# Performance work log

Measured on AMD Instinct MI355X. Metric: run time of the kernel, lower is better.

Reference implementation:

```python
import jax, jax.numpy as jnp
import numpy as np
from jax import lax

K = 3
STRIDE = 1
PAD = 1


def setup_inputs() -> dict:
    key = jax.random.key(0)
    k1, k2, k3, k4 = jax.random.split(key, 4)
    x = jax.random.normal(k1, (8, 64, 128, 128), dtype=jnp.float32)
    # offset conv params (trained-state stand-in; module inits to 0, which is degenerate)
    w_off = jax.random.normal(k2, (2 * K * K, 64, K, K), dtype=jnp.float32) * 0.01
    b_off = jax.random.normal(k3, (2 * K * K,), dtype=jnp.float32) * 0.01
    w_dcn = jax.random.normal(k4, (64, 64, K, K), dtype=jnp.float32) * 0.05
    return {"x": x, "w_off": w_off, "b_off": b_off, "w_dcn": w_dcn}


def _deform_conv(x, offset, weight):
    # x: [B,C,H,W]; offset: [B,2*K*K,Ho,Wo] interleaved (dy,dx) per kernel tap;
    # weight: [Cout,Cin,K,K]. Matches torchvision.ops.deform_conv2d semantics (groups=1).
    B, C, H, W = x.shape
    Cout = weight.shape[0]
    KK = K * K
    Ho = (H + 2 * PAD - K) // STRIDE + 1
    Wo = (W + 2 * PAD - K) // STRIDE + 1
    off = offset.reshape(B, KK, 2, Ho, Wo)
    ky = (jnp.arange(KK) // K).astype(x.dtype)
    kx = (jnp.arange(KK) % K).astype(x.dtype)
    base_y = (jnp.arange(Ho) * STRIDE - PAD).astype(x.dtype)
    base_x = (jnp.arange(Wo) * STRIDE - PAD).astype(x.dtype)
    # sampling coords per (batch, kernel tap, output y, output x)
    py = base_y[None, None, :, None] + ky[None, :, None, None] + off[:, :, 0]  # [B,KK,Ho,Wo]
    px = base_x[None, None, None, :] + kx[None, :, None, None] + off[:, :, 1]
    y0 = jnp.floor(py)
    x0 = jnp.floor(px)
    dy = py - y0
    dx = px - x0
    y0i = y0.astype(jnp.int32)
    x0i = x0.astype(jnp.int32)
    flat = x.reshape(B, C, H * W)

    def gather(yi, xi):
        valid = (yi >= 0) & (yi < H) & (xi >= 0) & (xi < W)
        idx = (jnp.clip(yi, 0, H - 1) * W + jnp.clip(xi, 0, W - 1)).reshape(B, -1)
        g = jax.vmap(lambda f, i: f[:, i])(flat, idx)  # [B,C,KK*Ho*Wo]
        return g.reshape(B, C, KK, Ho, Wo) * valid.reshape(B, 1, KK, Ho, Wo).astype(x.dtype)

    w00 = ((1 - dy) * (1 - dx))[:, None]  # [B,1,KK,Ho,Wo]
    w01 = ((1 - dy) * dx)[:, None]
    w10 = (dy * (1 - dx))[:, None]
    w11 = (dy * dx)[:, None]
    vals = (gather(y0i, x0i) * w00 + gather(y0i, x0i + 1) * w01
            + gather(y0i + 1, x0i) * w10 + gather(y0i + 1, x0i + 1) * w11)
    return jnp.einsum('bckhw,ock->bohw', vals, weight.reshape(Cout, C, KK))


def reference(x, w_off, b_off, w_dcn):
    offset = lax.conv_general_dilated(
        x, w_off, window_strides=(STRIDE, STRIDE),
        padding=((PAD, PAD), (PAD, PAD)),
        dimension_numbers=('NCHW', 'OIHW', 'NCHW')) + b_off[None, :, None, None]
    return _deform_conv(x, offset, w_dcn)
```

## Files before the change

kernel.cpp:

```cpp
#include <hip/hip_runtime.h>
#include <cmath>

#define BATCH 8
#define CIN   64
#define HH    128
#define WW    128
#define COUT  64
#define KKT   9
#define NOFF  18
#define PIX   16
#define NPX   32
#define KTOT  576
#define WROWS 6
#define WCOLS 24
#define NSAMP (NPX*KKT)
#define KH3   192

typedef __bf16 bf16x8 __attribute__((ext_vector_type(8)));
typedef float  f32x4  __attribute__((ext_vector_type(4)));
typedef float  f32x2  __attribute__((ext_vector_type(2)));
typedef unsigned int u32;
typedef u32    u32x4  __attribute__((ext_vector_type(4)));

__device__ __bf16 g_wb[18 * 4 * 4 * 16 * 8];
__device__ __bf16 g_wboff[18 * 2 * 4 * 16 * 8];

__global__ __launch_bounds__(256)
void prep_w(const float* __restrict__ w_dcn, const float* __restrict__ w_off) {
    const int idx = blockIdx.x * 256 + threadIdx.x;
    if (idx < 18 * 4 * 4 * 16 * 8) {
        const int e  = idx & 7;
        const int lr = (idx >> 3) & 15;
        const int lg = (idx >> 7) & 3;
        const int w  = (idx >> 9) & 3;
        const int kb = idx >> 11;
        const int cout = w * 16 + lr;
        const int k  = kb * 32 + lg * 8 + e;
        const int kk = k >> 6, ci = k & 63;
        g_wb[idx] = (__bf16)w_dcn[cout * KTOT + ci * KKT + kk];
    } else {
        const int j  = idx - 18 * 4 * 4 * 16 * 8;
        const int e  = j & 7;
        const int lr = (j >> 3) & 15;
        const int lg = (j >> 7) & 3;
        const int nt = (j >> 9) & 1;
        const int kb = j >> 10;
        const int oc = nt * 16 + lr;
        const int k  = kb * 32 + lg * 8 + e;
        const int kk = k >> 6, ci = k & 63;
        g_wboff[j] = (oc < NOFF) ? (__bf16)w_off[oc * KTOT + ci * KKT + kk] : (__bf16)0.f;
    }
}

static __device__ __forceinline__ f32x2 unpk(u32 v) {
    f32x2 r;
    r.x = __builtin_bit_cast(float, v << 16);
    r.y = __builtin_bit_cast(float, v & 0xffff0000u);
    return r;
}

__global__ __launch_bounds__(256)
void deform_fused(const float* __restrict__ x,
                  const float* __restrict__ b_off,
                  float* __restrict__ out) {
    __shared__ __align__(16) __bf16 s_xw[WROWS * WCOLS * 64];
    __shared__ __align__(16) __bf16 s_vals[NPX * KH3];
    __shared__ float s_off[NPX * NOFF];
    __shared__ int   s_yx[NSAMP];
    __shared__ float s_bw[NSAMP][4];
    __shared__ int   s_fast[NSAMP];

    const int blk   = blockIdx.x;
    const int wtile = blk % (WW / PIX);
    const int r0    = ((blk / (WW / PIX)) % (HH / 2)) * 2;
    const int b     = blk / ((WW / PIX) * (HH / 2));
    const int wbase = wtile * PIX;
    const int tid   = threadIdx.x;
    const int wid   = tid >> 6;
    const int lane  = tid & 63;
    const int lr    = lane & 15;
    const int lg    = lane >> 4;

    const float* __restrict__ xb = x + (size_t)b * CIN * HH * WW;
    const bool interior = (r0 >= 2) & (r0 <= HH - 4) & (wtile >= 1) & (wtile <= (WW / PIX) - 2);

    for (int t = tid; t < 6 * 64 * WROWS; t += 256) {
        const int c  = t % 6;
        const int ci = (t / 6) & 63;
        const int yr = t / 384;
        const int y  = r0 - 2 + yr;
        const int xs = wbase - 4 + c * 4;
        float v0 = 0.f, v1 = 0.f, v2 = 0.f, v3 = 0.f;
        if (interior) {
            const float* __restrict__ rp = xb + (size_t)ci * (HH * WW) + y * WW + xs;
            const f32x4 v = *(const f32x4*)rp;
            v0 = v[0]; v1 = v[1]; v2 = v[2]; v3 = v[3];
        } else if (y >= 0 && y < HH) {
            const float* __restrict__ rp = xb + (size_t)ci * (HH * WW) + y * WW + xs;
            if (xs >= 0 && xs <= WW - 4) {
                const f32x4 v = *(const f32x4*)rp;
                v0 = v[0]; v1 = v[1]; v2 = v[2]; v3 = v[3];
            } else {
                if (xs + 0 >= 0 && xs + 0 < WW) v0 = rp[0];
                if (xs + 1 >= 0 && xs + 1 < WW) v1 = rp[1];
                if (xs + 2 >= 0 && xs + 2 < WW) v2 = rp[2];
                if (xs + 3 >= 0 && xs + 3 < WW) v3 = rp[3];
            }
        }
        const int eb = ((yr * WCOLS + c * 4) << 6) + ci;
        s_xw[(eb + 0 * 64) ^ (((c * 4 + 0) & 7) << 3)] = (__bf16)v0;
        s_xw[(eb + 1 * 64) ^ (((c * 4 + 1) & 7) << 3)] = (__bf16)v1;
        s_xw[(eb + 2 * 64) ^ (((c * 4 + 2) & 7) << 3)] = (__bf16)v2;
        s_xw[(eb + 3 * 64) ^ (((c * 4 + 3) & 7) << 3)] = (__bf16)v3;
    }
    __syncthreads();

    {
        const int pg = wid >> 1;
        const int nt = wid & 1;
        f32x4 acc = {0.f, 0.f, 0.f, 0.f};
        #pragma unroll
        for (int kb = 0; kb < 18; ++kb) {
            const int kbase = kb * 32 + lg * 8;
            const int kk    = kbase >> 6;
            const int ci0   = kbase & 63;
            const int yr    = pg + kk / 3 + 1;
            const int xr    = lr + kk % 3 + 3;
            const int elem  = (((yr * WCOLS + xr) << 6) + ci0) ^ ((xr & 7) << 3);
            const bf16x8 a  = *(const bf16x8*)&s_xw[elem];
            const bf16x8 bb = *(const bf16x8*)&g_wboff[(((kb * 2 + nt) * 4 + lg) * 16 + lr) * 8];
            acc = __builtin_amdgcn_mfma_f32_16x16x32_bf16(a, bb, acc, 0, 0, 0);
        }
        const int oc = nt * 16 + lr;
        if (oc < NOFF) {
            const float bias = b_off[oc];
            #pragma unroll
            for (int r = 0; r < 4; ++r)
                s_off[(pg * 16 + lg * 4 + r) * NOFF + oc] = acc[r] + bias;
        }
    }
    __syncthreads();

    for (int m = tid; m < NSAMP; m += 256) {
        const int p  = m / KKT;
        const int kk = m - p * KKT;
        const int hp = r0 + (p >> 4);
        const int wo = wbase + (p & 15);
        const float py = (float)(hp - 1 + kk / 3) + s_off[p * NOFF + 2 * kk + 0];
        const float px = (float)(wo - 1 + kk % 3) + s_off[p * NOFF + 2 * kk + 1];
        const float fy = floorf(py), fx = floorf(px);
        const int y0 = (int)fy, x0 = (int)fx;
        const float dy = py - fy, dx = px - fx;
        s_yx[m] = (y0 << 16) | (x0 & 0xffff);
        s_fast[m] = (y0 >= r0 - 2) & (y0 <= r0 + 2) &
                    (x0 >= wbase - 4) & (x0 <= wbase + 18);
        s_bw[m][0] = (1.f - dy) * (1.f - dx);
        s_bw[m][1] = (1.f - dy) * dx;
        s_bw[m][2] = dy * (1.f - dx);
        s_bw[m][3] = dy * dx;
    }
    __syncthreads();

    auto run_task = [&](int m, int p, int kkl, int c8) {
        const int yx = s_yx[m];
        const int y0 = yx >> 16;
        const int x0 = (int)(short)(yx & 0xffff);
        const f32x4 w = *(const f32x4*)&s_bw[m][0];
        bf16x8 o;
        if (s_fast[m]) {
            const int yr  = y0 - (r0 - 2);
            const int xr  = x0 - (wbase - 4);
            const int e00 = ((yr * WCOLS + xr) << 6) + c8;
            const int sw0 = (xr & 7) << 3;
            const int sw1 = ((xr + 1) & 7) << 3;
            const u32x4 u00 = *(const u32x4*)&s_xw[e00 ^ sw0];
            const u32x4 u01 = *(const u32x4*)&s_xw[(e00 + 64) ^ sw1];
            const u32x4 u10 = *(const u32x4*)&s_xw[(e00 + WCOLS * 64) ^ sw0];
            const u32x4 u11 = *(const u32x4*)&s_xw[(e00 + (WCOLS + 1) * 64) ^ sw1];
            #pragma unroll
            for (int u = 0; u < 4; ++u) {
                f32x2 a = unpk(u00[u]) * w[0];
                a += unpk(u01[u]) * w[1];
                a += unpk(u10[u]) * w[2];
                a += unpk(u11[u]) * w[3];
                o[2 * u + 0] = (__bf16)a.x;
                o[2 * u + 1] = (__bf16)a.y;
            }
        } else {
            const int y1 = y0 + 1, x1 = x0 + 1;
            #pragma unroll
            for (int e = 0; e < 8; ++e) {
                const float* __restrict__ xc = xb + (size_t)(c8 + e) * (HH * WW);
                float v = 0.f;
                if (y0 >= 0 && y0 < HH) {
                    if (x0 >= 0 && x0 < WW) v += xc[y0 * WW + x0] * w[0];
                    if (x1 >= 0 && x1 < WW) v += xc[y0 * WW + x1] * w[1];
                }
                if (y1 >= 0 && y1 < HH) {
                    if (x0 >= 0 && x0 < WW) v += xc[y1 * WW + x0] * w[2];
                    if (x1 >= 0 && x1 < WW) v += xc[y1 * WW + x1] * w[3];
                }
                o[e] = (__bf16)v;
            }
        }
        const int ew = (kkl * 64 + c8) ^ ((p & 7) << 3);
        *(bf16x8*)&s_vals[p * KH3 + ew] = o;
    };

    f32x4 acc0 = {0.f, 0.f, 0.f, 0.f};
    f32x4 acc1 = {0.f, 0.f, 0.f, 0.f};
    const __bf16* __restrict__ bsrc = g_wb + (((size_t)wid * 4 + lg) * 16 + lr) * 8;

    #pragma unroll 1
    for (int pass = 0; pass < 3; ++pass) {
        for (int t = tid; t < 768; t += 256) {
            const int s3 = t >> 3, c8 = (t & 7) << 3;
            const int p = s3 / 3, kkl = s3 - p * 3;
            run_task(p * KKT + pass * 3 + kkl, p, kkl, c8);
        }
        __syncthreads();
        #pragma unroll
        for (int j = 0; j < 6; ++j) {
            const int kb = pass * 6 + j;
            const int ew = (j * 32 + lg * 8) ^ ((lr & 7) << 3);
            const bf16x8 bf = *(const bf16x8*)(bsrc + (size_t)kb * 2048);
            const bf16x8 a0 = *(const bf16x8*)&s_vals[lr * KH3 + ew];
            const bf16x8 a1 = *(const bf16x8*)&s_vals[(16 + lr) * KH3 + ew];
            acc0 = __builtin_amdgcn_mfma_f32_16x16x32_bf16(a0, bf, acc0, 0, 0, 0);
            acc1 = __builtin_amdgcn_mfma_f32_16x16x32_bf16(a1, bf, acc1, 0, 0, 0);
        }
        if (pass < 2) __syncthreads();
    }

    const int cout = wid * 16 + lr;
    const size_t ob0 = (((size_t)b * COUT + cout) * HH + r0) * WW + wbase + lg * 4;
    *(f32x4*)&out[ob0]      = acc0;
    *(f32x4*)&out[ob0 + WW] = acc1;
}

extern "C" void kernel_launch(void* const* d_in, const int* in_sizes, int n_in,
                              void* d_out, int out_size, void* d_ws, size_t ws_size,
                              hipStream_t stream) {
    const float* x     = (const float*)d_in[0];
    const float* w_off = (const float*)d_in[1];
    const float* b_off = (const float*)d_in[2];
    const float* w_dcn = (const float*)d_in[3];
    float* out = (float*)d_out;

    prep_w<<<216, 256, 0, stream>>>(w_dcn, w_off);

    const int nblocks = BATCH * (HH / 2) * (WW / PIX);
    deform_fused<<<nblocks, 256, 0, stream>>>(x, b_off, out);
}
```

Baseline: 70.00 us.

## Process four output rows per block with 512 threads to cut halo reloads

Each block now covers four output rows instead of two, using 512 threads. The loaded input window grows from 6 to 8 rows, so the halo overhead per output row shrinks and fewer blocks reload overlapping input. Waves split into cout tiles and row-pair halves for the MFMA stage. The per-sample fast-path flag is packed into the coordinate word, which removes one shared array. In exchange, shared memory per block grows and larger blocks may lower occupancy.

```diff
diff --git a/kernel.cpp b/kernel.cpp
--- a/kernel.cpp
+++ b/kernel.cpp
@@ -9,9 +9,10 @@
 #define KKT   9
 #define NOFF  18
 #define PIX   16
-#define NPX   32
+#define NROW  4
+#define NPX   64
 #define KTOT  576
-#define WROWS 6
+#define WROWS 8
 #define WCOLS 24
 #define NSAMP (NPX*KKT)
 #define KH3   192
@@ -59,7 +60,7 @@
     return r;
 }
 
-__global__ __launch_bounds__(256)
+__global__ __launch_bounds__(512)
 void deform_fused(const float* __restrict__ x,
                   const float* __restrict__ b_off,
                   float* __restrict__ out) {
@@ -68,12 +69,11 @@
     __shared__ float s_off[NPX * NOFF];
     __shared__ int   s_yx[NSAMP];
     __shared__ float s_bw[NSAMP][4];
-    __shared__ int   s_fast[NSAMP];
 
     const int blk   = blockIdx.x;
     const int wtile = blk % (WW / PIX);
-    const int r0    = ((blk / (WW / PIX)) % (HH / 2)) * 2;
-    const int b     = blk / ((WW / PIX) * (HH / 2));
+    const int r0    = ((blk / (WW / PIX)) % (HH / NROW)) * NROW;
+    const int b     = blk / ((WW / PIX) * (HH / NROW));
     const int wbase = wtile * PIX;
     const int tid   = threadIdx.x;
     const int wid   = tid >> 6;
@@ -82,9 +82,9 @@
     const int lg    = lane >> 4;
 
     const float* __restrict__ xb = x + (size_t)b * CIN * HH * WW;
-    const bool interior = (r0 >= 2) & (r0 <= HH - 4) & (wtile >= 1) & (wtile <= (WW / PIX) - 2);
-
-    for (int t = tid; t < 6 * 64 * WROWS; t += 256) {
+    const bool interior = (r0 >= 2) & (r0 <= HH - 6) & (wtile >= 1) & (wtile <= (WW / PIX) - 2);
+
+    for (int t = tid; t < 6 * 64 * WROWS; t += 512) {
         const int c  = t % 6;
         const int ci = (t / 6) & 63;
         const int yr = t / 384;
@@ -141,7 +141,7 @@
     }
     __syncthreads();
 
-    for (int m = tid; m < NSAMP; m += 256) {
+    for (int m = tid; m < NSAMP; m += 512) {
         const int p  = m / KKT;
         const int kk = m - p * KKT;
         const int hp = r0 + (p >> 4);
@@ -151,9 +151,9 @@
         const float fy = floorf(py), fx = floorf(px);
         const int y0 = (int)fy, x0 = (int)fx;
         const float dy = py - fy, dx = px - fx;
-        s_yx[m] = (y0 << 16) | (x0 & 0xffff);
-        s_fast[m] = (y0 >= r0 - 2) & (y0 <= r0 + 2) &
-                    (x0 >= wbase - 4) & (x0 <= wbase + 18);
+        const int fast = (y0 >= r0 - 2) & (y0 <= r0 + 4) &
+                         (x0 >= wbase - 4) & (x0 <= wbase + 18);
+        s_yx[m] = (y0 << 16) | (fast << 15) | (x0 & 0x7fff);
         s_bw[m][0] = (1.f - dy) * (1.f - dx);
         s_bw[m][1] = (1.f - dy) * dx;
         s_bw[m][2] = dy * (1.f - dx);
@@ -164,10 +164,10 @@
     auto run_task = [&](int m, int p, int kkl, int c8) {
         const int yx = s_yx[m];
         const int y0 = yx >> 16;
-        const int x0 = (int)(short)(yx & 0xffff);
+        const int x0 = (yx << 17) >> 17;
         const f32x4 w = *(const f32x4*)&s_bw[m][0];
         bf16x8 o;
-        if (s_fast[m]) {
+        if (yx & 0x8000) {
             const int yr  = y0 - (r0 - 2);
             const int xr  = x0 - (wbase - 4);
             const int e00 = ((yr * WCOLS + xr) << 6) + c8;
@@ -207,13 +207,17 @@
         *(bf16x8*)&s_vals[p * KH3 + ew] = o;
     };
 
+    const int ct = wid >> 1;
+    const int ph = wid & 1;
     f32x4 acc0 = {0.f, 0.f, 0.f, 0.f};
     f32x4 acc1 = {0.f, 0.f, 0.f, 0.f};
-    const __bf16* __restrict__ bsrc = g_wb + (((size_t)wid * 4 + lg) * 16 + lr) * 8;
+    const __bf16* __restrict__ bsrc = g_wb + (((size_t)ct * 4 + lg) * 16 + lr) * 8;
+    const int p0 = (ph * 2 + 0) * 16 + lr;
+    const int p1 = (ph * 2 + 1) * 16 + lr;
 
     #pragma unroll 1
     for (int pass = 0; pass < 3; ++pass) {
-        for (int t = tid; t < 768; t += 256) {
+        for (int t = tid; t < 1536; t += 512) {
             const int s3 = t >> 3, c8 = (t & 7) << 3;
             const int p = s3 / 3, kkl = s3 - p * 3;
             run_task(p * KKT + pass * 3 + kkl, p, kkl, c8);
@@ -224,16 +228,16 @@
             const int kb = pass * 6 + j;
             const int ew = (j * 32 + lg * 8) ^ ((lr & 7) << 3);
             const bf16x8 bf = *(const bf16x8*)(bsrc + (size_t)kb * 2048);
-            const bf16x8 a0 = *(const bf16x8*)&s_vals[lr * KH3 + ew];
-            const bf16x8 a1 = *(const bf16x8*)&s_vals[(16 + lr) * KH3 + ew];
+            const bf16x8 a0 = *(const bf16x8*)&s_vals[p0 * KH3 + ew];
+            const bf16x8 a1 = *(const bf16x8*)&s_vals[p1 * KH3 + ew];
             acc0 = __builtin_amdgcn_mfma_f32_16x16x32_bf16(a0, bf, acc0, 0, 0, 0);
             acc1 = __builtin_amdgcn_mfma_f32_16x16x32_bf16(a1, bf, acc1, 0, 0, 0);
         }
         if (pass < 2) __syncthreads();
     }
 
-    const int cout = wid * 16 + lr;
-    const size_t ob0 = (((size_t)b * COUT + cout) * HH + r0) * WW + wbase + lg * 4;
+    const int cout = ct * 16 + lr;
+    const size_t ob0 = (((size_t)b * COUT + cout) * HH + r0 + ph * 2) * WW + wbase + lg * 4;
     *(f32x4*)&out[ob0]      = acc0;
     *(f32x4*)&out[ob0 + WW] = acc1;
 }
@@ -249,6 +253,6 @@
 
     prep_w<<<216, 256, 0, stream>>>(w_dcn, w_off);
 
-    const int nblocks = BATCH * (HH / 2) * (WW / PIX);
-    deform_fused<<<nblocks, 256, 0, stream>>>(x, b_off, out);
-}
+    const int nblocks = BATCH * (HH / NROW) * (WW / PIX);
+    deform_fused<<<nblocks, 512, 0, stream>>>(x, b_off, out);
+}
```

Measured after the change: 71.07 us. No clear change (+1.5%).

## Double-buffer sampled values to overlap bilinear gather with MFMA passes

Applied to the files above, without the earlier changes.

Splits the sampled-value staging buffer into two shared buffers so the gather for the next pass runs while the MFMA GEMM consumes the previous one, which removes one barrier per pass. Each thread now handles 16 channels per task instead of 8, and the fast-path flag is packed into the coordinate word so the separate s_fast array is gone. Shared memory use grows by one extra vals buffer, which may reduce occupancy, and the larger per-thread task raises register pressure and leaves load imbalance (384 tasks over 256 threads).

```diff
diff --git a/kernel.cpp b/kernel.cpp
--- a/kernel.cpp
+++ b/kernel.cpp
@@ -64,11 +64,11 @@
                   const float* __restrict__ b_off,
                   float* __restrict__ out) {
     __shared__ __align__(16) __bf16 s_xw[WROWS * WCOLS * 64];
-    __shared__ __align__(16) __bf16 s_vals[NPX * KH3];
+    __shared__ __align__(16) __bf16 s_valsA[NPX * KH3];
+    __shared__ __align__(16) __bf16 s_valsB[NPX * KH3];
     __shared__ float s_off[NPX * NOFF];
     __shared__ int   s_yx[NSAMP];
     __shared__ float s_bw[NSAMP][4];
-    __shared__ int   s_fast[NSAMP];
 
     const int blk   = blockIdx.x;
     const int wtile = blk % (WW / PIX);
@@ -151,9 +151,9 @@
         const float fy = floorf(py), fx = floorf(px);
         const int y0 = (int)fy, x0 = (int)fx;
         const float dy = py - fy, dx = px - fx;
-        s_yx[m] = (y0 << 16) | (x0 & 0xffff);
-        s_fast[m] = (y0 >= r0 - 2) & (y0 <= r0 + 2) &
-                    (x0 >= wbase - 4) & (x0 <= wbase + 18);
+        const int fast = (y0 >= r0 - 2) & (y0 <= r0 + 2) &
+                         (x0 >= wbase - 4) & (x0 <= wbase + 18);
+        s_yx[m] = (y0 << 16) | (fast << 15) | (x0 & 0x7fff);
         s_bw[m][0] = (1.f - dy) * (1.f - dx);
         s_bw[m][1] = (1.f - dy) * dx;
         s_bw[m][2] = dy * (1.f - dx);
@@ -161,76 +161,98 @@
     }
     __syncthreads();
 
-    auto run_task = [&](int m, int p, int kkl, int c8) {
+    auto run_task16 = [&](int m, int p, int kkl, int c16, __bf16* __restrict__ dst) {
         const int yx = s_yx[m];
         const int y0 = yx >> 16;
-        const int x0 = (int)(short)(yx & 0xffff);
+        const int x0 = (yx << 17) >> 17;
         const f32x4 w = *(const f32x4*)&s_bw[m][0];
-        bf16x8 o;
-        if (s_fast[m]) {
-            const int yr  = y0 - (r0 - 2);
-            const int xr  = x0 - (wbase - 4);
-            const int e00 = ((yr * WCOLS + xr) << 6) + c8;
-            const int sw0 = (xr & 7) << 3;
-            const int sw1 = ((xr + 1) & 7) << 3;
-            const u32x4 u00 = *(const u32x4*)&s_xw[e00 ^ sw0];
-            const u32x4 u01 = *(const u32x4*)&s_xw[(e00 + 64) ^ sw1];
-            const u32x4 u10 = *(const u32x4*)&s_xw[(e00 + WCOLS * 64) ^ sw0];
-            const u32x4 u11 = *(const u32x4*)&s_xw[(e00 + (WCOLS + 1) * 64) ^ sw1];
+        if (yx & 0x8000) {
+            const int yr   = y0 - (r0 - 2);
+            const int xr   = x0 - (wbase - 4);
+            const int b00  = (yr * WCOLS + xr) << 6;
+            const int sw0  = (xr & 7) << 3;
+            const int sw1  = ((xr + 1) & 7) << 3;
             #pragma unroll
-            for (int u = 0; u < 4; ++u) {
-                f32x2 a = unpk(u00[u]) * w[0];
-                a += unpk(u01[u]) * w[1];
-                a += unpk(u10[u]) * w[2];
-                a += unpk(u11[u]) * w[3];
-                o[2 * u + 0] = (__bf16)a.x;
-                o[2 * u + 1] = (__bf16)a.y;
+            for (int h = 0; h < 2; ++h) {
+                const int c8  = c16 + h * 8;
+                const int e00 = b00 + c8;
+                const u32x4 u00 = *(const u32x4*)&s_xw[e00 ^ sw0];
+                const u32x4 u01 = *(const u32x4*)&s_xw[(e00 + 64) ^ sw1];
+                const u32x4 u10 = *(const u32x4*)&s_xw[(e00 + WCOLS * 64) ^ sw0];
+                const u32x4 u11 = *(const u32x4*)&s_xw[(e00 + (WCOLS + 1) * 64) ^ sw1];
+                bf16x8 o;
+                #pragma unroll
+                for (int u = 0; u < 4; ++u) {
+                    f32x2 a = unpk(u00[u]) * w[0];
+                    a += unpk(u01[u]) * w[1];
+                    a += unpk(u10[u]) * w[2];
+                    a += unpk(u11[u]) * w[3];
+                    o[2 * u + 0] = (__bf16)a.x;
+                    o[2 * u + 1] = (__bf16)a.y;
+                }
+                const int ew = (kkl * 64 + c8) ^ ((p & 7) << 3);
+                *(bf16x8*)&dst[p * KH3 + ew] = o;
             }
         } else {
             const int y1 = y0 + 1, x1 = x0 + 1;
             #pragma unroll
-            for (int e = 0; e < 8; ++e) {
-                const float* __restrict__ xc = xb + (size_t)(c8 + e) * (HH * WW);
-                float v = 0.f;
-                if (y0 >= 0 && y0 < HH) {
-                    if (x0 >= 0 && x0 < WW) v += xc[y0 * WW + x0] * w[0];
-                    if (x1 >= 0 && x1 < WW) v += xc[y0 * WW + x1] * w[1];
+            for (int h = 0; h < 2; ++h) {
+                const int c8 = c16 + h * 8;
+                bf16x8 o;
+                #pragma unroll
+                for (int e = 0; e < 8; ++e) {
+                    const float* __restrict__ xc = xb + (size_t)(c8 + e) * (HH * WW);
+                    float v = 0.f;
+                    if (y0 >= 0 && y0 < HH) {
+                        if (x0 >= 0 && x0 < WW) v += xc[y0 * WW + x0] * w[0];
+                        if (x1 >= 0 && x1 < WW) v += xc[y0 * WW + x1] * w[1];
+                    }
+                    if (y1 >= 0 && y1 < HH) {
+                        if (x0 >= 0 && x0 < WW) v += xc[y1 * WW + x0] * w[2];
+                        if (x1 >= 0 && x1 < WW) v += xc[y1 * WW + x1] * w[3];
+                    }
+                    o[e] = (__bf16)v;
                 }
-                if (y1 >= 0 && y1 < HH) {
-                    if (x0 >= 0 && x0 < WW) v += xc[y1 * WW + x0] * w[2];
-                    if (x1 >= 0 && x1 < WW) v += xc[y1 * WW + x1] * w[3];
-                }
-                o[e] = (__bf16)v;
+                const int ew = (kkl * 64 + c8) ^ ((p & 7) << 3);
+                *(bf16x8*)&dst[p * KH3 + ew] = o;
             }
         }
-        const int ew = (kkl * 64 + c8) ^ ((p & 7) << 3);
-        *(bf16x8*)&s_vals[p * KH3 + ew] = o;
+    };
+
+    auto do_tasks = [&](int pass, __bf16* __restrict__ dst) {
+        for (int t = tid; t < 384; t += 256) {
+            const int s3 = t >> 2, c16 = (t & 3) << 4;
+            const int p = s3 / 3, kkl = s3 - p * 3;
+            run_task16(p * KKT + pass * 3 + kkl, p, kkl, c16, dst);
+        }
     };
 
     f32x4 acc0 = {0.f, 0.f, 0.f, 0.f};
     f32x4 acc1 = {0.f, 0.f, 0.f, 0.f};
     const __bf16* __restrict__ bsrc = g_wb + (((size_t)wid * 4 + lg) * 16 + lr) * 8;
 
-    #pragma unroll 1
-    for (int pass = 0; pass < 3; ++pass) {
-        for (int t = tid; t < 768; t += 256) {
-            const int s3 = t >> 3, c8 = (t & 7) << 3;
-            const int p = s3 / 3, kkl = s3 - p * 3;
-            run_task(p * KKT + pass * 3 + kkl, p, kkl, c8);
-        }
-        __syncthreads();
+    auto do_gemm = [&](int pass, const __bf16* __restrict__ src) {
         #pragma unroll
         for (int j = 0; j < 6; ++j) {
             const int kb = pass * 6 + j;
             const int ew = (j * 32 + lg * 8) ^ ((lr & 7) << 3);
             const bf16x8 bf = *(const bf16x8*)(bsrc + (size_t)kb * 2048);
-            const bf16x8 a0 = *(const bf16x8*)&s_vals[lr * KH3 + ew];
-            const bf16x8 a1 = *(const bf16x8*)&s_vals[(16 + lr) * KH3 + ew];
+            const bf16x8 a0 = *(const bf16x8*)&src[lr * KH3 + ew];
+            const bf16x8 a1 = *(const bf16x8*)&src[(16 + lr) * KH3 + ew];
             acc0 = __builtin_amdgcn_mfma_f32_16x16x32_bf16(a0, bf, acc0, 0, 0, 0);
             acc1 = __builtin_amdgcn_mfma_f32_16x16x32_bf16(a1, bf, acc1, 0, 0, 0);
         }
-        if (pass < 2) __syncthreads();
-    }
+    };
+
+    do_tasks(0, s_valsA);
+    __syncthreads();
+    do_tasks(1, s_valsB);
+    do_gemm(0, s_valsA);
+    __syncthreads();
+    do_tasks(2, s_valsA);
+    do_gemm(1, s_valsB);
+    __syncthreads();
+    do_gemm(2, s_valsA);
 
     const int cout = wid * 16 + lr;
     const size_t ob0 = (((size_t)b * COUT + cout) * HH + r0) * WW + wbase + lg * 4;
```

Measured after the change: 78.26 us. 11.8% more time.

## Build MFMA A-fragments in registers, split K across waves, drop staging buffer

Applied to the files above, without the earlier changes.

Each lane now computes its bilinear samples straight into the MFMA A-operand registers instead of writing them to a shared staging buffer and reading them back. The four waves are reorganised as 2 pixel groups × 2 K-halves, each computing all 64 output channels, and the partial sums are reduced through shared memory at the end. This removes the three-pass staging loop with its barriers and the s_vals/s_fast shared arrays, packs the fast-path flag into the coordinate word, and adds an occupancy hint of 5 blocks per CU. In exchange, each sample is computed by a single thread with less parallelism spread, and the added reduction step plus the register pressure from the launch-bounds hint could cost performance.

```diff
diff --git a/kernel.cpp b/kernel.cpp
--- a/kernel.cpp
+++ b/kernel.cpp
@@ -14,7 +14,6 @@
 #define WROWS 6
 #define WCOLS 24
 #define NSAMP (NPX*KKT)
-#define KH3   192
 
 typedef __bf16 bf16x8 __attribute__((ext_vector_type(8)));
 typedef float  f32x4  __attribute__((ext_vector_type(4)));
@@ -59,16 +58,14 @@
     return r;
 }
 
-__global__ __launch_bounds__(256)
+__global__ __launch_bounds__(256, 5)
 void deform_fused(const float* __restrict__ x,
                   const float* __restrict__ b_off,
                   float* __restrict__ out) {
     __shared__ __align__(16) __bf16 s_xw[WROWS * WCOLS * 64];
-    __shared__ __align__(16) __bf16 s_vals[NPX * KH3];
     __shared__ float s_off[NPX * NOFF];
     __shared__ int   s_yx[NSAMP];
     __shared__ float s_bw[NSAMP][4];
-    __shared__ int   s_fast[NSAMP];
 
     const int blk   = blockIdx.x;
     const int wtile = blk % (WW / PIX);
@@ -151,9 +148,9 @@
         const float fy = floorf(py), fx = floorf(px);
         const int y0 = (int)fy, x0 = (int)fx;
         const float dy = py - fy, dx = px - fx;
-        s_yx[m] = (y0 << 16) | (x0 & 0xffff);
-        s_fast[m] = (y0 >= r0 - 2) & (y0 <= r0 + 2) &
-                    (x0 >= wbase - 4) & (x0 <= wbase + 18);
+        const int fast = (y0 >= r0 - 2) & (y0 <= r0 + 2) &
+                         (x0 >= wbase - 4) & (x0 <= wbase + 18);
+        s_yx[m] = (y0 << 16) | (fast << 15) | (x0 & 0x7fff);
         s_bw[m][0] = (1.f - dy) * (1.f - dx);
         s_bw[m][1] = (1.f - dy) * dx;
         s_bw[m][2] = dy * (1.f - dx);
@@ -161,16 +158,29 @@
     }
     __syncthreads();
 
-    auto run_task = [&](int m, int p, int kkl, int c8) {
+    const int kh  = wid >> 1;
+    const int pg  = wid & 1;
+    const int pix = pg * 16 + lr;
+    const int ci0 = kh * 32 + lg * 8;
+
+    f32x4 acc0 = {0.f, 0.f, 0.f, 0.f};
+    f32x4 acc1 = {0.f, 0.f, 0.f, 0.f};
+    f32x4 acc2 = {0.f, 0.f, 0.f, 0.f};
+    f32x4 acc3 = {0.f, 0.f, 0.f, 0.f};
+
+    #pragma unroll
+    for (int j = 0; j < 9; ++j) {
+        const int kb = 2 * j + kh;
+        const int m  = pix * KKT + j;
         const int yx = s_yx[m];
         const int y0 = yx >> 16;
-        const int x0 = (int)(short)(yx & 0xffff);
+        const int x0 = (yx << 17) >> 17;
         const f32x4 w = *(const f32x4*)&s_bw[m][0];
-        bf16x8 o;
-        if (s_fast[m]) {
+        bf16x8 afrag;
+        if (yx & 0x8000) {
             const int yr  = y0 - (r0 - 2);
             const int xr  = x0 - (wbase - 4);
-            const int e00 = ((yr * WCOLS + xr) << 6) + c8;
+            const int e00 = ((yr * WCOLS + xr) << 6) + ci0;
             const int sw0 = (xr & 7) << 3;
             const int sw1 = ((xr + 1) & 7) << 3;
             const u32x4 u00 = *(const u32x4*)&s_xw[e00 ^ sw0];
@@ -183,14 +193,14 @@
                 a += unpk(u01[u]) * w[1];
                 a += unpk(u10[u]) * w[2];
                 a += unpk(u11[u]) * w[3];
-                o[2 * u + 0] = (__bf16)a.x;
-                o[2 * u + 1] = (__bf16)a.y;
+                afrag[2 * u + 0] = (__bf16)a.x;
+                afrag[2 * u + 1] = (__bf16)a.y;
             }
         } else {
             const int y1 = y0 + 1, x1 = x0 + 1;
             #pragma unroll
             for (int e = 0; e < 8; ++e) {
-                const float* __restrict__ xc = xb + (size_t)(c8 + e) * (HH * WW);
+                const float* __restrict__ xc = xb + (size_t)(ci0 + e) * (HH * WW);
                 float v = 0.f;
                 if (y0 >= 0 && y0 < HH) {
                     if (x0 >= 0 && x0 < WW) v += xc[y0 * WW + x0] * w[0];
@@ -200,42 +210,40 @@
                     if (x0 >= 0 && x0 < WW) v += xc[y1 * WW + x0] * w[2];
                     if (x1 >= 0 && x1 < WW) v += xc[y1 * WW + x1] * w[3];
                 }
-                o[e] = (__bf16)v;
+                afrag[e] = (__bf16)v;
             }
         }
-        const int ew = (kkl * 64 + c8) ^ ((p & 7) << 3);
-        *(bf16x8*)&s_vals[p * KH3 + ew] = o;
-    };
-
-    f32x4 acc0 = {0.f, 0.f, 0.f, 0.f};
-    f32x4 acc1 = {0.f, 0.f, 0.f, 0.f};
-    const __bf16* __restrict__ bsrc = g_wb + (((size_t)wid * 4 + lg) * 16 + lr) * 8;
-
-    #pragma unroll 1
-    for (int pass = 0; pass < 3; ++pass) {
-        for (int t = tid; t < 768; t += 256) {
-            const int s3 = t >> 3, c8 = (t & 7) << 3;
-            const int p = s3 / 3, kkl = s3 - p * 3;
-            run_task(p * KKT + pass * 3 + kkl, p, kkl, c8);
-        }
-        __syncthreads();
-        #pragma unroll
-        for (int j = 0; j < 6; ++j) {
-            const int kb = pass * 6 + j;
-            const int ew = (j * 32 + lg * 8) ^ ((lr & 7) << 3);
-            const bf16x8 bf = *(const bf16x8*)(bsrc + (size_t)kb * 2048);
-            const bf16x8 a0 = *(const bf16x8*)&s_vals[lr * KH3 + ew];
-            const bf16x8 a1 = *(const bf16x8*)&s_vals[(16 + lr) * KH3 + ew];
-            acc0 = __builtin_amdgcn_mfma_f32_16x16x32_bf16(a0, bf, acc0, 0, 0, 0);
-            acc1 = __builtin_amdgcn_mfma_f32_16x16x32_bf16(a1, bf, acc1, 0, 0, 0);
-        }
-        if (pass < 2) __syncthreads();
-    }
-
-    const int cout = wid * 16 + lr;
-    const size_t ob0 = (((size_t)b * COUT + cout) * HH + r0) * WW + wbase + lg * 4;
-    *(f32x4*)&out[ob0]      = acc0;
-    *(f32x4*)&out[ob0 + WW] = acc1;
+        const __bf16* __restrict__ bp = g_wb + (size_t)kb * 2048 + lg * 128 + lr * 8;
+        acc0 = __builtin_amdgcn_mfma_f32_16x16x32_bf16(afrag, *(const bf16x8*)(bp + 0 * 512), acc0, 0, 0, 0);
+        acc1 = __builtin_amdgcn_mfma_f32_16x16x32_bf16(afrag, *(const bf16x8*)(bp + 1 * 512), acc1, 0, 0, 0);
+        acc2 = __builtin_amdgcn_mfma_f32_16x16x32_bf16(afrag, *(const bf16x8*)(bp + 2 * 512), acc2, 0, 0, 0);
+        acc3 = __builtin_amdgcn_mfma_f32_16x16x32_bf16(afrag, *(const bf16x8*)(bp + 3 * 512), acc3, 0, 0, 0);
+    }
+    __syncthreads();
+
+    f32x4* red = (f32x4*)s_xw;
+    if (kh == 1) {
+        const int base = (pg * 64 + lane) * 5;
+        red[base + 0] = acc0;
+        red[base + 1] = acc1;
+        red[base + 2] = acc2;
+        red[base + 3] = acc3;
+    }
+    __syncthreads();
+    if (kh == 0) {
+        const int base = (pg * 64 + lane) * 5;
+        const f32x4 t0 = red[base + 0];
+        const f32x4 t1 = red[base + 1];
+        const f32x4 t2 = red[base + 2];
+        const f32x4 t3 = red[base + 3];
+        acc0 += t0; acc1 += t1; acc2 += t2; acc3 += t3;
+        const size_t orow = ((size_t)b * COUT + lr) * HH + r0 + pg;
+        const size_t ocol = wbase + lg * 4;
+        *(f32x4*)&out[(orow +  0 * (size_t)HH) * WW + ocol] = acc0;
+        *(f32x4*)&out[(orow + 16 * (size_t)HH) * WW + ocol] = acc1;
+        *(f32x4*)&out[(orow + 32 * (size_t)HH) * WW + ocol] = acc2;
+        *(f32x4*)&out[(orow + 48 * (size_t)HH) * WW + ocol] = acc3;
+    }
 }
 
 extern "C" void kernel_launch(void* const* d_in, const int* in_sizes, int n_in,
```

Result: slower. 71.72 us (+2.5%).
